# Kernel optimization log

Measured on AMD Instinct MI355X. Metric: run time of the kernel, lower is better.

## Reference

```python
import jax, jax.numpy as jnp
import numpy as np

THRESHOLD_FRAC = 0.1  # default `threshold` kwarg in RingLoss.forward


def _l2_normalize(x):
    # matches torch.nn.functional.normalize(x, p=2, dim=1, eps=1e-12)
    n = jnp.linalg.norm(x, axis=1, keepdims=True)
    return x / jnp.maximum(n, 1e-12)


def setup_inputs() -> dict:
    key = jax.random.key(0)
    k1, k2, k3 = jax.random.split(key, 3)
    N, D = 4096, 512
    h1 = jax.random.normal(k1, (N, D), dtype=jnp.float32)
    h2 = jax.random.normal(k2, (N, D), dtype=jnp.float32)
    y = jax.random.randint(k3, (N,), 0, 100)  # class labels
    tau = jnp.asarray(0.5, dtype=jnp.float32)  # contrastive temperature
    return {"h1": h1, "h2": h2, "y": y, "tau": tau}


def reference(h1, h2, y, tau):
    # NOTE: in the original module, `y` is only used to build false_neg_mask /
    # false_neg_cnt, which are dead values (never used in the returned loss).
    # The loss itself depends only on h1, h2, tau, threshold.
    N = h1.shape[0]
    t = int(N * THRESHOLD_FRAC)  # static ring cutoff

    h1n = _l2_normalize(h1)
    h2n = _l2_normalize(h2)

    s12 = h1n @ h2n.T  # [N, N] cross-view similarity
    s11 = h1n @ h1n.T  # [N, N]
    s22 = h2n @ h2n.T  # [N, N]

    neg1 = jnp.concatenate([s11, s12], axis=1)    # [N, 2N]
    neg2 = jnp.concatenate([s12.T, s22], axis=1)  # [N, 2N]

    # sort descending per row, keep the middle "ring" [t : 2N - t]
    neg1 = jnp.sort(neg1, axis=1)[:, ::-1][:, t:2 * N - t]
    neg2 = jnp.sort(neg2, axis=1)[:, ::-1][:, t:2 * N - t]

    f = lambda x: jnp.exp(x / tau)
    pos = f(jnp.diagonal(s12))      # [N]
    n1 = f(neg1).sum(axis=1)        # [N]
    n2 = f(neg2).sum(axis=1)        # [N]

    loss = 0.5 * (-jnp.log(pos / n1) - jnp.log(pos / n2))
    return loss.mean()
```

## Files before the change

kernel.cpp:

```cpp
#include <hip/hip_runtime.h>


typedef unsigned short u16;
typedef __bf16 bf16x8 __attribute__((ext_vector_type(8)));
typedef float f32x4 __attribute__((ext_vector_type(4)));
typedef u16 u16x8 __attribute__((ext_vector_type(8)));

#define NROW 8192
#define NHALF 4096
#define DIM 512
#define RING_T 409
#define NB 256
#define BSCALE 121.904762f

__device__ inline u16 f2bf(float f) {
  unsigned u = __builtin_bit_cast(unsigned, f);
  unsigned r = (u + 0x7fffu + ((u >> 16) & 1u)) >> 16;
  return (u16)r;
}
__device__ inline float bf2f(u16 h) {
  unsigned u = ((unsigned)h) << 16;
  return __builtin_bit_cast(float, u);
}
__device__ inline int bucket_of(float v) {
  int b = (int)((v + 1.05f) * BSCALE);
  return b < 0 ? 0 : (b > (NB - 1) ? (NB - 1) : b);
}

__device__ inline float block_sum(float x, volatile float* s4, int t) {
  #pragma unroll
  for (int off = 32; off > 0; off >>= 1) x += __shfl_down(x, off);
  __syncthreads();
  if ((t & 63) == 0) s4[t >> 6] = x;
  __syncthreads();
  return s4[0] + s4[1] + s4[2] + s4[3];
}

__global__ __launch_bounds__(256) void normalize_k(const float* __restrict__ h1,
                                                   const float* __restrict__ h2,
                                                   u16* __restrict__ G) {
  const int r = blockIdx.x;
  const int t = threadIdx.x;
  const float* src = (r < NHALF) ? (h1 + (size_t)r * DIM) : (h2 + (size_t)(r - NHALF) * DIM);
  float2 x = *(const float2*)(src + (t << 1));
  __shared__ float s4[4];
  float tot = block_sum(x.x * x.x + x.y * x.y, s4, t);
  float scale = 1.0f / fmaxf(sqrtf(tot), 1e-12f);
  unsigned pk = (unsigned)f2bf(x.x * scale) | ((unsigned)f2bf(x.y * scale) << 16);
  *(unsigned*)(G + (size_t)r * DIM + (t << 1)) = pk;
}

__global__ __launch_bounds__(256) void diag_k(const float* __restrict__ h1,
                                              const float* __restrict__ h2,
                                              float* __restrict__ accums) {
  const int i = blockIdx.x, t = threadIdx.x;
  float2 a = *(const float2*)(h1 + (size_t)i * DIM + (t << 1));
  float2 b = *(const float2*)(h2 + (size_t)i * DIM + (t << 1));
  __shared__ float s4[4];
  float S11 = block_sum(a.x * a.x + a.y * a.y, s4, t);
  float S22 = block_sum(b.x * b.x + b.y * b.y, s4, t);
  float S12 = block_sum(a.x * b.x + a.y * b.y, s4, t);
  if (t == 0) {
    float d = S12 / (fmaxf(sqrtf(S11), 1e-12f) * fmaxf(sqrtf(S22), 1e-12f));
    atomicAdd(&accums[1], d);
  }
}

#define BK 32

__device__ inline void gload_lds16(const u16* g, u16* lds_base) {
  __builtin_amdgcn_global_load_lds(
      (const __attribute__((address_space(1))) void*)g,
      (__attribute__((address_space(3))) void*)lds_base, 16, 0, 0);
}

__global__ __launch_bounds__(256) void gram_gemm(const u16* __restrict__ G,
                                                 u16* __restrict__ S,
                                                 int row0) {
  __shared__ u16 As[128 * BK];
  __shared__ u16 Bs[128 * BK];
  const int t = threadIdx.x;
  const int lane = t & 63;
  const int wave = t >> 6;
  const int wm = wave >> 1, wn = wave & 1;
  const int brow = row0 + (blockIdx.y << 7), bcol = blockIdx.x << 7;
  const int fr = lane & 15, fg = lane >> 4;

  const int srow = lane >> 2;
  const int scol = (lane & 3) << 3;
  const int chA0 = wave, chA1 = wave + 4;

  f32x4 acc[4][4] = {};

  for (int ks = 0; ks < DIM; ks += BK) {
    __syncthreads();
    gload_lds16(G + (size_t)(brow + (chA0 << 4) + srow) * DIM + ks + scol, As + (chA0 << 9));
    gload_lds16(G + (size_t)(brow + (chA1 << 4) + srow) * DIM + ks + scol, As + (chA1 << 9));
    gload_lds16(G + (size_t)(bcol + (chA0 << 4) + srow) * DIM + ks + scol, Bs + (chA0 << 9));
    gload_lds16(G + (size_t)(bcol + (chA1 << 4) + srow) * DIM + ks + scol, Bs + (chA1 << 9));
    __syncthreads();

    bf16x8 af[4], bfr[4];
    #pragma unroll
    for (int m = 0; m < 4; ++m)
      af[m] = __builtin_bit_cast(bf16x8,
          *(const u16x8*)(&As[(((wm << 6) + (m << 4) + fr) << 5) + (fg << 3)]));
    #pragma unroll
    for (int n = 0; n < 4; ++n)
      bfr[n] = __builtin_bit_cast(bf16x8,
          *(const u16x8*)(&Bs[(((wn << 6) + (n << 4) + fr) << 5) + (fg << 3)]));
    #pragma unroll
    for (int m = 0; m < 4; ++m)
      #pragma unroll
      for (int n = 0; n < 4; ++n)
        acc[m][n] = __builtin_amdgcn_mfma_f32_16x16x32_bf16(af[m], bfr[n], acc[m][n], 0, 0, 0);
  }

  #pragma unroll
  for (int m = 0; m < 4; ++m)
    #pragma unroll
    for (int n = 0; n < 4; ++n) {
      int lrow = (blockIdx.y << 7) + (wm << 6) + (m << 4) + (fg << 2);
      int col = bcol + (wn << 6) + (n << 4) + fr;
      #pragma unroll
      for (int j = 0; j < 4; ++j)
        S[(size_t)(lrow + j) * NROW + col] = f2bf(acc[m][n][j]);
    }
}

__global__ __launch_bounds__(256) void ring_k(const u16* __restrict__ S,
                                              const float* __restrict__ taup,
                                              float* __restrict__ accums) {
  __shared__ unsigned hist4[4 * NB];
  __shared__ unsigned cnt[NB];
  __shared__ unsigned sfx[NB];
  __shared__ unsigned wavetot[4];
  __shared__ float red[4 * 8];
  __shared__ int bhl[2];
  const int r = blockIdx.x, t = threadIdx.x;
  const int lane = t & 63, w = t >> 6;
  const float inv_tau = 1.0f / taup[0];

  #pragma unroll
  for (int k = 0; k < 4; ++k) hist4[t + (k << 8)] = 0;
  __syncthreads();

  float v[32];
  const u16* row = S + (size_t)r * NROW;
  #pragma unroll
  for (int q = 0; q < 4; ++q) {
    u16x8 u = *(const u16x8*)(row + (((q << 8) + t) << 3));
    #pragma unroll
    for (int j = 0; j < 8; ++j) v[(q << 3) + j] = bf2f(u[j]);
  }
  unsigned* myhist = &hist4[w << 8];
  #pragma unroll
  for (int i = 0; i < 32; ++i) atomicAdd(&myhist[bucket_of(v[i])], 1u);
  __syncthreads();

  unsigned c = hist4[t] + hist4[t + 256] + hist4[t + 512] + hist4[t + 768];
  cnt[t] = c;
  unsigned x = c;
  #pragma unroll
  for (int off = 1; off < 64; off <<= 1) {
    unsigned y = __shfl_down(x, off);
    if (lane + off < 64) x += y;
  }
  unsigned wt = __shfl(x, 0);
  if (lane == 0) wavetot[w] = wt;
  __syncthreads();
  unsigned hi = 0;
  #pragma unroll
  for (int k = 0; k < 4; ++k) hi += (k > w) ? wavetot[k] : 0u;
  sfx[t] = x + hi;
  __syncthreads();

  {
    unsigned ai = sfx[t];
    unsigned ae = (t < NB - 1) ? sfx[t + 1] : 0u;
    if (ai >= RING_T && ae < RING_T) bhl[0] = t;
    unsigned beq = NROW - ae;
    unsigned blt = NROW - ai;
    if (beq >= RING_T && blt < RING_T) bhl[1] = t;
  }
  __syncthreads();
  const int bh = bhl[0], bl = bhl[1];

  float eTot = 0, eAb = 0, eHi = 0, eBe = 0, eLo = 0;
  #pragma unroll
  for (int i = 0; i < 32; ++i) {
    float e = __expf(v[i] * inv_tau);
    int b = bucket_of(v[i]);
    eTot += e;
    eAb += (b > bh) ? e : 0.0f;
    eHi += (b == bh) ? e : 0.0f;
    eBe += (b < bl) ? e : 0.0f;
    eLo += (b == bl) ? e : 0.0f;
  }
  float acc5[5] = {eTot, eAb, eHi, eBe, eLo};
  #pragma unroll
  for (int q = 0; q < 5; ++q)
    #pragma unroll
    for (int off = 32; off > 0; off >>= 1) acc5[q] += __shfl_down(acc5[q], off);
  if (lane == 0)
    #pragma unroll
    for (int q = 0; q < 5; ++q) red[(w << 3) + q] = acc5[q];
  __syncthreads();

  if (t == 0) {
    float s5[5];
    #pragma unroll
    for (int q = 0; q < 5; ++q)
      s5[q] = red[q] + red[8 + q] + red[16 + q] + red[24 + q];
    unsigned cAb = (bh + 1 < NB) ? sfx[bh + 1] : 0u;
    unsigned cBe = NROW - sfx[bl];
    unsigned ch = cnt[bh], cl = cnt[bl];
    float sumTop = s5[1] + (ch ? (float)(RING_T - cAb) * (s5[2] / (float)ch) : 0.0f);
    float sumBot = s5[3] + (cl ? (float)(RING_T - cBe) * (s5[4] / (float)cl) : 0.0f);
    float n = s5[0] - sumTop - sumBot;
    atomicAdd(&accums[0], 0.5f * logf(n));
  }
}

__global__ void init_k(float* accums) {
  if (threadIdx.x < 2) accums[threadIdx.x] = 0.0f;
}

__global__ void final_k(const float* __restrict__ accums,
                        const float* __restrict__ taup,
                        float* __restrict__ out) {
  out[0] = (accums[0] - accums[1] / taup[0]) * (1.0f / (float)NHALF);
}

extern "C" void kernel_launch(void* const* d_in, const int* in_sizes, int n_in,
                              void* d_out, int out_size, void* d_ws, size_t ws_size,
                              hipStream_t stream) {
  const float* h1 = (const float*)d_in[0];
  const float* h2 = (const float*)d_in[1];
  const float* taup = (const float*)d_in[3];
  float* out = (float*)d_out;

  char* ws = (char*)d_ws;
  u16* G = (u16*)ws;
  float* accums = (float*)(ws + (size_t)8 * 1024 * 1024);
  u16* Schunk = (u16*)(ws + (size_t)8 * 1024 * 1024 + 256);

  size_t avail = (ws_size > (size_t)8 * 1024 * 1024 + 256)
                     ? ws_size - (size_t)8 * 1024 * 1024 - 256 : 0;
  long long rpc = (long long)(avail / ((size_t)NROW * 2));
  rpc = (rpc / 128) * 128;
  if (rpc < 128) rpc = 128;
  if (rpc > NROW) rpc = NROW;

  hipLaunchKernelGGL(init_k, dim3(1), dim3(64), 0, stream, accums);
  hipLaunchKernelGGL(normalize_k, dim3(NROW), dim3(256), 0, stream, h1, h2, G);
  hipLaunchKernelGGL(diag_k, dim3(NHALF), dim3(256), 0, stream, h1, h2, accums);

  for (int r0 = 0; r0 < NROW; r0 += (int)rpc) {
    int rows = (int)((r0 + rpc <= NROW) ? rpc : (NROW - r0));
    hipLaunchKernelGGL(gram_gemm, dim3(64, rows >> 7), dim3(256), 0, stream,
                       G, Schunk, r0);
    hipLaunchKernelGGL(ring_k, dim3(rows), dim3(256), 0, stream,
                       Schunk, taup, accums);
  }

  hipLaunchKernelGGL(final_k, dim3(1), dim3(1), 0, stream, accums, taup, out);
}
```

Baseline: 333.2 us.

## Process one row per wavefront in ring kernel with fused exp-sum histogram

Restructures the ring kernel so each wavefront handles a whole row instead of each block handling one row. It accumulates per-bucket counts and per-bucket exp sums in shared memory in one pass, dropping the block-wide barriers and the second bucket/exp pass. The boundary-bucket interpolation now comes from wave-level suffix scans over the bucket sums. This cuts __syncthreads and duplicate work, but adds float atomics in LDS and more registers per thread from holding 16 vector loads.

```diff
diff --git a/kernel.cpp b/kernel.cpp
--- a/kernel.cpp
+++ b/kernel.cpp
@@ -131,95 +131,84 @@
 __global__ __launch_bounds__(256) void ring_k(const u16* __restrict__ S,
                                               const float* __restrict__ taup,
                                               float* __restrict__ accums) {
-  __shared__ unsigned hist4[4 * NB];
-  __shared__ unsigned cnt[NB];
-  __shared__ unsigned sfx[NB];
-  __shared__ unsigned wavetot[4];
-  __shared__ float red[4 * 8];
-  __shared__ int bhl[2];
-  const int r = blockIdx.x, t = threadIdx.x;
-  const int lane = t & 63, w = t >> 6;
-  const float inv_tau = 1.0f / taup[0];
-
-  #pragma unroll
-  for (int k = 0; k < 4; ++k) hist4[t + (k << 8)] = 0;
-  __syncthreads();
-
-  float v[32];
+  __shared__ unsigned cnt[4][2][NB];
+  __shared__ float esm[4][2][NB];
+  const int t = threadIdx.x;
+  const int w = t >> 6, lane = t & 63;
+  const int r = (blockIdx.x << 2) + w;
+  const float se = (1.0f / taup[0]) * 1.44269504f;
+
+  #pragma unroll
+  for (int i = 0; i < 8; ++i) {
+    cnt[w][0][(i << 6) + lane + 0] = 0u;
+    cnt[w][1][(i << 6) + lane + 0] = 0u;
+    esm[w][0][(i << 6) + lane + 0] = 0.0f;
+    esm[w][1][(i << 6) + lane + 0] = 0.0f;
+  }
+  asm volatile("s_waitcnt lgkmcnt(0)" ::: "memory");
+
   const u16* row = S + (size_t)r * NROW;
-  #pragma unroll
-  for (int q = 0; q < 4; ++q) {
-    u16x8 u = *(const u16x8*)(row + (((q << 8) + t) << 3));
-    #pragma unroll
-    for (int j = 0; j < 8; ++j) v[(q << 3) + j] = bf2f(u[j]);
-  }
-  unsigned* myhist = &hist4[w << 8];
-  #pragma unroll
-  for (int i = 0; i < 32; ++i) atomicAdd(&myhist[bucket_of(v[i])], 1u);
-  __syncthreads();
-
-  unsigned c = hist4[t] + hist4[t + 256] + hist4[t + 512] + hist4[t + 768];
-  cnt[t] = c;
-  unsigned x = c;
+  u16x8 u[16];
+  #pragma unroll
+  for (int q = 0; q < 16; ++q)
+    u[q] = *(const u16x8*)(row + (q << 9) + (lane << 3));
+
+  unsigned* myc = &cnt[w][lane >> 5][0];
+  float* mye = &esm[w][lane >> 5][0];
+  #pragma unroll
+  for (int q = 0; q < 16; ++q)
+    #pragma unroll
+    for (int j = 0; j < 8; ++j) {
+      float v = bf2f(u[q][j]);
+      int b = bucket_of(v);
+      float e = __builtin_amdgcn_exp2f(v * se);
+      atomicAdd(&myc[b], 1u);
+      unsafeAtomicAdd(&mye[b], e);
+    }
+  asm volatile("s_waitcnt lgkmcnt(0)" ::: "memory");
+
+  uint4 ca = *(const uint4*)&cnt[w][0][lane << 2];
+  uint4 cb = *(const uint4*)&cnt[w][1][lane << 2];
+  float4 ea = *(const float4*)&esm[w][0][lane << 2];
+  float4 eb = *(const float4*)&esm[w][1][lane << 2];
+  unsigned g0 = ca.x + cb.x, g1 = ca.y + cb.y, g2 = ca.z + cb.z, g3 = ca.w + cb.w;
+  float f0 = ea.x + eb.x, f1 = ea.y + eb.y, f2 = ea.z + eb.z, f3 = ea.w + eb.w;
+
+  unsigned ls3 = g3, ls2 = g2 + ls3, ls1 = g1 + ls2, ls0 = g0 + ls1;
+  float es3 = f3, es2 = f2 + es3, es1 = f1 + es2, es0 = f0 + es1;
+
+  unsigned x = ls0; float ex = es0;
   #pragma unroll
   for (int off = 1; off < 64; off <<= 1) {
     unsigned y = __shfl_down(x, off);
-    if (lane + off < 64) x += y;
-  }
-  unsigned wt = __shfl(x, 0);
-  if (lane == 0) wavetot[w] = wt;
-  __syncthreads();
-  unsigned hi = 0;
-  #pragma unroll
-  for (int k = 0; k < 4; ++k) hi += (k > w) ? wavetot[k] : 0u;
-  sfx[t] = x + hi;
-  __syncthreads();
-
-  {
-    unsigned ai = sfx[t];
-    unsigned ae = (t < NB - 1) ? sfx[t + 1] : 0u;
-    if (ai >= RING_T && ae < RING_T) bhl[0] = t;
-    unsigned beq = NROW - ae;
-    unsigned blt = NROW - ai;
-    if (beq >= RING_T && blt < RING_T) bhl[1] = t;
-  }
-  __syncthreads();
-  const int bh = bhl[0], bl = bhl[1];
-
-  float eTot = 0, eAb = 0, eHi = 0, eBe = 0, eLo = 0;
-  #pragma unroll
-  for (int i = 0; i < 32; ++i) {
-    float e = __expf(v[i] * inv_tau);
-    int b = bucket_of(v[i]);
-    eTot += e;
-    eAb += (b > bh) ? e : 0.0f;
-    eHi += (b == bh) ? e : 0.0f;
-    eBe += (b < bl) ? e : 0.0f;
-    eLo += (b == bl) ? e : 0.0f;
-  }
-  float acc5[5] = {eTot, eAb, eHi, eBe, eLo};
-  #pragma unroll
-  for (int q = 0; q < 5; ++q)
-    #pragma unroll
-    for (int off = 32; off > 0; off >>= 1) acc5[q] += __shfl_down(acc5[q], off);
-  if (lane == 0)
-    #pragma unroll
-    for (int q = 0; q < 5; ++q) red[(w << 3) + q] = acc5[q];
-  __syncthreads();
-
-  if (t == 0) {
-    float s5[5];
-    #pragma unroll
-    for (int q = 0; q < 5; ++q)
-      s5[q] = red[q] + red[8 + q] + red[16 + q] + red[24 + q];
-    unsigned cAb = (bh + 1 < NB) ? sfx[bh + 1] : 0u;
-    unsigned cBe = NROW - sfx[bl];
-    unsigned ch = cnt[bh], cl = cnt[bl];
-    float sumTop = s5[1] + (ch ? (float)(RING_T - cAb) * (s5[2] / (float)ch) : 0.0f);
-    float sumBot = s5[3] + (cl ? (float)(RING_T - cBe) * (s5[4] / (float)cl) : 0.0f);
-    float n = s5[0] - sumTop - sumBot;
-    atomicAdd(&accums[0], 0.5f * logf(n));
-  }
+    float z = __shfl_down(ex, off);
+    if (lane + off < 64) { x += y; ex += z; }
+  }
+  const unsigned T = x - ls0;
+  const float TE = ex - es0;
+  const float eTot = __shfl(ex, 0);
+
+  float tb = 0.0f;
+  #pragma unroll
+  for (int j = 0; j < 4; ++j) {
+    unsigned gj = (j == 0) ? g0 : (j == 1) ? g1 : (j == 2) ? g2 : g3;
+    unsigned lsj = (j == 0) ? ls0 : (j == 1) ? ls1 : (j == 2) ? ls2 : ls3;
+    float fj = (j == 0) ? f0 : (j == 1) ? f1 : (j == 2) ? f2 : f3;
+    float esj = (j == 0) ? es0 : (j == 1) ? es1 : (j == 2) ? es2 : es3;
+    unsigned sf = lsj + T;
+    unsigned nsf = sf - gj;
+    float ef = esj + TE;
+    if (sf >= RING_T && nsf < RING_T)
+      tb += (ef - fj) + (float)(RING_T - nsf) * (fj / (float)gj);
+    unsigned below_eq = NROW - nsf;
+    unsigned below = NROW - sf;
+    if (below_eq >= RING_T && below < RING_T)
+      tb += (eTot - ef) + (float)(RING_T - below) * (fj / (float)gj);
+  }
+  #pragma unroll
+  for (int off = 32; off > 0; off >>= 1) tb += __shfl_down(tb, off);
+
+  if (lane == 0) atomicAdd(&accums[0], 0.5f * __logf(eTot - tb));
 }
 
 __global__ void init_k(float* accums) {
@@ -260,7 +249,7 @@
     int rows = (int)((r0 + rpc <= NROW) ? rpc : (NROW - r0));
     hipLaunchKernelGGL(gram_gemm, dim3(64, rows >> 7), dim3(256), 0, stream,
                        G, Schunk, r0);
-    hipLaunchKernelGGL(ring_k, dim3(rows), dim3(256), 0, stream,
+    hipLaunchKernelGGL(ring_k, dim3(rows >> 2), dim3(256), 0, stream,
                        Schunk, taup, accums);
   }
 
```

Result: slower. 589.4 us (+76.9%).
